# Kernel optimization log

Measured on AMD Instinct MI355X. Metric: run time of the kernel, lower is better.

## Reference

```python
import jax, jax.numpy as jnp
import numpy as np

B, S, D, H = 64, 512, 1024, 1024


def setup_inputs() -> dict:
    key = jax.random.key(0)
    k1, k2, k3 = jax.random.split(key, 3)
    scale = 1.0 / np.sqrt(H)
    U = jax.random.normal(k1, (B, S, D), dtype=jnp.float32)
    W_ih = jax.random.normal(k2, (3 * H, D), dtype=jnp.float32) * scale
    W_hh = jax.random.normal(k3, (3 * H, H), dtype=jnp.float32) * scale
    b_ih = jnp.zeros((3 * H,), dtype=jnp.float32)
    b_hh = jnp.zeros((3 * H,), dtype=jnp.float32)
    return {"U": U, "W_ih": W_ih, "W_hh": W_hh, "b_ih": b_ih, "b_hh": b_hh}


def _gru_scan(U, W_ih, W_hh, b_ih, b_hh):
    # Precompute input-side gate projections for all timesteps: [B,S,3H]
    x_gates = jnp.einsum('bsd,gd->bsg', U, W_ih) + b_ih
    x_gates = jnp.transpose(x_gates, (1, 0, 2))  # [S,B,3H] for scan
    h0 = jnp.zeros((U.shape[0], W_hh.shape[1]), dtype=U.dtype)

    def step(h, xg):
        hg = h @ W_hh.T + b_hh  # [B,3H]
        xr, xz, xn = jnp.split(xg, 3, axis=-1)
        hr, hz, hn = jnp.split(hg, 3, axis=-1)
        r = jax.nn.sigmoid(xr + hr)
        z = jax.nn.sigmoid(xz + hz)
        n = jnp.tanh(xn + r * hn)
        h_new = (1.0 - z) * n + z * h
        return h_new, None

    h_final, _ = jax.lax.scan(step, h0, x_gates)
    return h_final  # [B,H]


def reference(U, W_ih, W_hh, b_ih, b_hh):
    # Dropout p=0.0 (eval-equivalent) -> identity, omitted.
    return _gru_scan(U, W_ih, W_hh, b_ih, b_hh)
```

## Files before the change

### kernel.cpp

```cpp
#include <hip/hip_runtime.h>

#define S_LEN 512
#define BATCH 64
#define HDIM  1024
#define GDIM  3072

typedef __attribute__((ext_vector_type(8))) short bf16x8;
typedef __attribute__((ext_vector_type(4))) float f32x4;
typedef __attribute__((ext_vector_type(4))) unsigned short u16x4;

__device__ inline unsigned short f2bf(float f) {
  unsigned u = __builtin_bit_cast(unsigned, f);
  u += 0x7fffu + ((u >> 16) & 1u);
  return (unsigned short)(u >> 16);
}
__device__ inline float bf2f(unsigned short h) {
  unsigned u = ((unsigned)h) << 16;
  return __builtin_bit_cast(float, u);
}
__device__ inline bf16x8 pack8(float4 a, float4 b) {
  bf16x8 r;
  r[0] = (short)f2bf(a.x); r[1] = (short)f2bf(a.y);
  r[2] = (short)f2bf(a.z); r[3] = (short)f2bf(a.w);
  r[4] = (short)f2bf(b.x); r[5] = (short)f2bf(b.y);
  r[6] = (short)f2bf(b.z); r[7] = (short)f2bf(b.w);
  return r;
}

__global__ __launch_bounds__(256, 2) void xg_gemm(
    const float* __restrict__ U, const float* __restrict__ Wih,
    const float* __restrict__ bih, unsigned short* __restrict__ xg) {
  __shared__ bf16x8 Asub[512];
  __shared__ bf16x8 Bsub[512];

  const int bid = blockIdx.x;
  const int nt = bid % 24;
  const int mt = bid / 24;
  const int tid = threadIdx.x;
  const int wave = tid >> 6, lane = tid & 63;
  const int q = lane >> 4, l15 = lane & 15;
  const int wm = wave >> 1, wn = wave & 1;

  const int srow = tid >> 1, shalf = tid & 1;
  const int arow = mt * 128 + srow;
  const float* Ag = U + ((size_t)(arow & 63) * S_LEN + (arow >> 6)) * HDIM + shalf * 16;
  const float* Bg = Wih + (size_t)(nt * 128 + srow) * HDIM + shalf * 16;
  const int sw = (srow >> 1) & 3;
  const int slot0 = srow * 4 + ((shalf * 2) ^ sw);
  const int slot1 = srow * 4 + ((shalf * 2 + 1) ^ sw);

  f32x4 acc[4][4];
#pragma unroll
  for (int i = 0; i < 4; ++i)
#pragma unroll
    for (int j = 0; j < 4; ++j) acc[i][j] = (f32x4){0.f, 0.f, 0.f, 0.f};

  for (int kk = 0; kk < 32; ++kk) {
    const float4* ap = (const float4*)(Ag + kk * 32);
    float4 a0 = ap[0], a1 = ap[1], a2 = ap[2], a3 = ap[3];
    const float4* bp = (const float4*)(Bg + kk * 32);
    float4 b0 = bp[0], b1 = bp[1], b2 = bp[2], b3 = bp[3];
    Asub[slot0] = pack8(a0, a1);
    Asub[slot1] = pack8(a2, a3);
    Bsub[slot0] = pack8(b0, b1);
    Bsub[slot1] = pack8(b2, b3);
    __syncthreads();
    bf16x8 af[4], bfr[4];
#pragma unroll
    for (int i = 0; i < 4; ++i) {
      int ar = wm * 64 + i * 16 + l15;
      af[i] = Asub[ar * 4 + (q ^ ((ar >> 1) & 3))];
      int br = wn * 64 + i * 16 + l15;
      bfr[i] = Bsub[br * 4 + (q ^ ((br >> 1) & 3))];
    }
#pragma unroll
    for (int i = 0; i < 4; ++i)
#pragma unroll
      for (int j = 0; j < 4; ++j)
        acc[i][j] = __builtin_amdgcn_mfma_f32_16x16x32_bf16(af[i], bfr[j], acc[i][j], 0, 0, 0);
    __syncthreads();
  }

#pragma unroll
  for (int j = 0; j < 4; ++j) {
    int gcol = nt * 128 + wn * 64 + j * 16 + l15;
    float bias = bih[gcol];
#pragma unroll
    for (int i = 0; i < 4; ++i) {
      int rbase = mt * 128 + wm * 64 + i * 16 + q * 4;
      int s = rbase >> 6;
      int b0i = rbase & 63;
      u16x4 pk;
#pragma unroll
      for (int r = 0; r < 4; ++r) pk[r] = f2bf(acc[i][j][r] + bias);
      *(u16x4*)(xg + ((size_t)s * GDIM + gcol) * BATCH + b0i) = pk;
    }
  }
}

__global__ __launch_bounds__(512, 1) void gru_scan(
    const float* __restrict__ Whh, const float* __restrict__ bhh,
    const unsigned short* __restrict__ xg, unsigned short* __restrict__ hbuf,
    unsigned int* __restrict__ flags, float* __restrict__ out) {
  __shared__ unsigned short hls[8 * 8192];
  __shared__ float bh_lds[3][16];

  const int p = blockIdx.x;
  const int j0 = p * 16;
  const int tid = threadIdx.x;
  const int w = tid >> 6, lane = tid & 63;
  const int q = lane >> 4, l15 = lane & 15;
  const int k0 = w * 128;
  const int cb = tid >> 2;
  const int cmq = (tid & 3) * 4;

  const int srow0 = lane >> 4;
  const int sc = lane & 15;

  bf16x8 wf[3][4];
#pragma unroll
  for (int g = 0; g < 3; ++g) {
    const float* wrow = Whh + ((size_t)g * HDIM + j0 + l15) * HDIM + k0;
#pragma unroll
    for (int kk = 0; kk < 4; ++kk) {
      const float4* wp = (const float4*)(wrow + kk * 32 + q * 8);
      wf[g][kk] = pack8(wp[0], wp[1]);
    }
  }
  if (tid < 48) bh_lds[tid >> 4][tid & 15] = bhh[(tid >> 4) * HDIM + j0 + (tid & 15)];
  __syncthreads();

  float4 hv = {0.f, 0.f, 0.f, 0.f};

  unsigned short xq[3][4];
  if (tid < 256) {
#pragma unroll
    for (int g = 0; g < 3; ++g)
#pragma unroll
      for (int r = 0; r < 4; ++r)
        xq[g][r] = xg[((size_t)g * HDIM + j0 + cmq + r) * BATCH + cb];
  }

  const size_t HS = (size_t)BATCH * HDIM;
  int dead = 0;

  for (int t = 0; t < S_LEN; ++t) {
    const unsigned short* hcur = hbuf + (size_t)(t & 1) * HS;
    unsigned short* hnxt = hbuf + (size_t)((t + 1) & 1) * HS;

    {
      const unsigned short* gb = hcur + (size_t)srow0 * HDIM + k0 + sc * 8;
      const unsigned short *g0 = gb,            *g1 = gb + 4 * HDIM,
                           *g2 = gb + 8 * HDIM, *g3 = gb + 12 * HDIM,
                           *g4 = gb + 16 * HDIM,*g5 = gb + 20 * HDIM,
                           *g6 = gb + 24 * HDIM,*g7 = gb + 28 * HDIM;
      bf16x8 v0, v1, v2, v3, v4, v5, v6, v7;
      asm volatile(
          "global_load_dwordx4 %0, %8, off sc0 sc1\n\t"
          "global_load_dwordx4 %1, %9, off sc0 sc1\n\t"
          "global_load_dwordx4 %2, %10, off sc0 sc1\n\t"
          "global_load_dwordx4 %3, %11, off sc0 sc1\n\t"
          "global_load_dwordx4 %4, %12, off sc0 sc1\n\t"
          "global_load_dwordx4 %5, %13, off sc0 sc1\n\t"
          "global_load_dwordx4 %6, %14, off sc0 sc1\n\t"
          "global_load_dwordx4 %7, %15, off sc0 sc1"
          : "=&v"(v0), "=&v"(v1), "=&v"(v2), "=&v"(v3),
            "=&v"(v4), "=&v"(v5), "=&v"(v6), "=&v"(v7)
          : "v"(g0), "v"(g1), "v"(g2), "v"(g3),
            "v"(g4), "v"(g5), "v"(g6), "v"(g7));
      const unsigned short *g8 = gb + 32 * HDIM, *g9 = gb + 36 * HDIM,
                           *gA = gb + 40 * HDIM, *gB = gb + 44 * HDIM,
                           *gC = gb + 48 * HDIM, *gD = gb + 52 * HDIM,
                           *gE = gb + 56 * HDIM, *gF = gb + 60 * HDIM;
      bf16x8 v8, v9, vA, vB, vC, vD, vE, vF;
      asm volatile(
          "global_load_dwordx4 %0, %8, off sc0 sc1\n\t"
          "global_load_dwordx4 %1, %9, off sc0 sc1\n\t"
          "global_load_dwordx4 %2, %10, off sc0 sc1\n\t"
          "global_load_dwordx4 %3, %11, off sc0 sc1\n\t"
          "global_load_dwordx4 %4, %12, off sc0 sc1\n\t"
          "global_load_dwordx4 %5, %13, off sc0 sc1\n\t"
          "global_load_dwordx4 %6, %14, off sc0 sc1\n\t"
          "global_load_dwordx4 %7, %15, off sc0 sc1"
          : "=&v"(v8), "=&v"(v9), "=&v"(vA), "=&v"(vB),
            "=&v"(vC), "=&v"(vD), "=&v"(vE), "=&v"(vF)
          : "v"(g8), "v"(g9), "v"(gA), "v"(gB),
            "v"(gC), "v"(gD), "v"(gE), "v"(gF));

#define STW(J, VV)                                                        \
      {                                                                   \
        const int row_ = srow0 + 4 * (J);                                 \
        const int c2_ = (sc & 8) | ((sc ^ row_) & 7);                     \
        *(bf16x8*)&hls[w * 8192 + row_ * 128 + c2_ * 8] = (VV);           \
      }
      asm volatile("s_waitcnt vmcnt(8)" ::: "memory");
      __builtin_amdgcn_sched_barrier(0);
      STW(0, v0) STW(1, v1) STW(2, v2) STW(3, v3)
      STW(4, v4) STW(5, v5) STW(6, v6) STW(7, v7)
      asm volatile("s_waitcnt vmcnt(0)" ::: "memory");
      __builtin_amdgcn_sched_barrier(0);
      STW(8, v8) STW(9, v9) STW(10, vA) STW(11, vB)
      STW(12, vC) STW(13, vD) STW(14, vE) STW(15, vF)
#undef STW
    }

    f32x4 acc[3][4];
#pragma unroll
    for (int g = 0; g < 3; ++g)
#pragma unroll
      for (int bt = 0; bt < 4; ++bt) acc[g][bt] = (f32x4){0.f, 0.f, 0.f, 0.f};

#pragma unroll
    for (int kk = 0; kk < 4; ++kk) {
      const int c = kk * 4 + q;
      bf16x8 hB[4];
#pragma unroll
      for (int bt = 0; bt < 4; ++bt) {
        const int row = bt * 16 + l15;
        const int c2 = (c & 8) | ((c ^ row) & 7);
        hB[bt] = *(const bf16x8*)&hls[w * 8192 + row * 128 + c2 * 8];
      }
#pragma unroll
      for (int g = 0; g < 3; ++g) {
        acc[g][0] = __builtin_amdgcn_mfma_f32_16x16x32_bf16(wf[g][kk], hB[0], acc[g][0], 0, 0, 0);
        acc[g][1] = __builtin_amdgcn_mfma_f32_16x16x32_bf16(wf[g][kk], hB[1], acc[g][1], 0, 0, 0);
        acc[g][2] = __builtin_amdgcn_mfma_f32_16x16x32_bf16(wf[g][kk], hB[2], acc[g][2], 0, 0, 0);
        acc[g][3] = __builtin_amdgcn_mfma_f32_16x16x32_bf16(wf[g][kk], hB[3], acc[g][3], 0, 0, 0);
      }
    }
    __builtin_amdgcn_sched_barrier(0);

    {
      float* pw = (float*)&hls[w * 8192];
      asm volatile("" : "+v"(pw));
#pragma unroll
      for (int g = 0; g < 3; ++g)
#pragma unroll
        for (int bt = 0; bt < 4; ++bt)
#pragma unroll
          for (int r = 0; r < 4; ++r)
            pw[(g * 16 + q * 4 + r) * 66 + bt * 16 + l15] = acc[g][bt][r];
    }
    __syncthreads();

    if (tid < 256) {
      u16x4 pk;
#pragma unroll
      for (int r = 0; r < 4; ++r) {
        int m = cmq + r;
        float hr = bh_lds[0][m], hz = bh_lds[1][m], hn = bh_lds[2][m];
#pragma unroll
        for (int ww = 0; ww < 8; ++ww) {
          const float* pp = (const float*)&hls[ww * 8192];
          hr += pp[( 0 + m) * 66 + cb];
          hz += pp[(16 + m) * 66 + cb];
          hn += pp[(32 + m) * 66 + cb];
        }
        float xr = bf2f(xq[0][r]), xz = bf2f(xq[1][r]), xn = bf2f(xq[2][r]);
        float rr = 1.f / (1.f + __expf(-(xr + hr)));
        float zz = 1.f / (1.f + __expf(-(xz + hz)));
        float ex = __expf(2.f * (xn + rr * hn));
        float nn = 1.f - 2.f / (ex + 1.f);
        float hold = (r == 0) ? hv.x : (r == 1) ? hv.y : (r == 2) ? hv.z : hv.w;
        float hnew = (1.f - zz) * nn + zz * hold;
        if (r == 0) hv.x = hnew; else if (r == 1) hv.y = hnew; else if (r == 2) hv.z = hnew; else hv.w = hnew;
        pk[r] = f2bf(hnew);
      }
      if (t + 1 < S_LEN) {
        __hip_atomic_store((unsigned long long*)(hnxt + (size_t)cb * HDIM + j0 + cmq),
                           __builtin_bit_cast(unsigned long long, pk),
                           __ATOMIC_RELAXED, __HIP_MEMORY_SCOPE_AGENT);
      }
    }
    __syncthreads();

    if (t + 1 < S_LEN) {
      if (tid == 448)
        __hip_atomic_store(&flags[p], (unsigned)(t + 1),
                           __ATOMIC_RELAXED, __HIP_MEMORY_SCOPE_AGENT);
      if (tid < 256) {
#pragma unroll
        for (int g = 0; g < 3; ++g)
#pragma unroll
          for (int r = 0; r < 4; ++r)
            xq[g][r] = xg[((size_t)(t + 1) * GDIM + g * HDIM + j0 + cmq + r) * BATCH + cb];
      }
      if (tid >= 448 && !dead) {
        const unsigned int* fp = flags + (tid & 63);
        const unsigned want = (unsigned)(t + 1);
        unsigned spins = 0;
        while (__hip_atomic_load(fp, __ATOMIC_RELAXED, __HIP_MEMORY_SCOPE_AGENT)
               < want) {
          __builtin_amdgcn_s_sleep(1);
          if (++spins > 50000000u) { dead = 1; break; }
        }
      }
      __syncthreads();
    }
  }

  if (tid < 256)
    *(float4*)(out + (size_t)cb * HDIM + j0 + cmq) = hv;
}

extern "C" void kernel_launch(void* const* d_in, const int* in_sizes, int n_in,
                              void* d_out, int out_size, void* d_ws, size_t ws_size,
                              hipStream_t stream) {
  const float* U   = (const float*)d_in[0];
  const float* Wih = (const float*)d_in[1];
  const float* Whh = (const float*)d_in[2];
  const float* bih = (const float*)d_in[3];
  const float* bhh = (const float*)d_in[4];
  float* out = (float*)d_out;

  char* ws = (char*)d_ws;
  const size_t XG_BYTES = (size_t)S_LEN * GDIM * BATCH * 2;
  unsigned short* xg   = (unsigned short*)ws;
  unsigned short* hbuf = (unsigned short*)(ws + XG_BYTES);
  const size_t H_BYTES = (size_t)2 * BATCH * HDIM * 2;
  unsigned int* flags  = (unsigned int*)(ws + XG_BYTES + H_BYTES);

  hipMemsetAsync(ws + XG_BYTES, 0, H_BYTES + 256, stream);

  hipLaunchKernelGGL(xg_gemm, dim3((32768 / 128) * (GDIM / 128)), dim3(256), 0, stream,
                     U, Wih, bih, xg);
  hipLaunchKernelGGL(gru_scan, dim3(64), dim3(512), 0, stream,
                     Whh, bhh, xg, hbuf, flags, out);
}
```

Before: 3.595 ms.

## Replace flag-based step barrier with tagged fp32 hidden-state polling

Adds a new scan kernel that keeps the hidden state in fp32 with the step index embedded in the low 8 mantissa bits. Consumers validate each loaded vector's tag and reload until it matches, which removes the separate flag/barrier synchronization between blocks each timestep. This trades twice the hidden-state traffic and a small precision loss in the low mantissa bits for lower inter-block sync latency. The old flag-based kernel stays as a fallback when the workspace is too small.

```diff
diff --git a/kernel.cpp b/kernel.cpp
--- a/kernel.cpp
+++ b/kernel.cpp
@@ -24,6 +24,14 @@
   r[2] = (short)f2bf(a.z); r[3] = (short)f2bf(a.w);
   r[4] = (short)f2bf(b.x); r[5] = (short)f2bf(b.y);
   r[6] = (short)f2bf(b.z); r[7] = (short)f2bf(b.w);
+  return r;
+}
+__device__ inline bf16x8 pack8v(f32x4 a, f32x4 b) {
+  bf16x8 r;
+  r[0] = (short)f2bf(a[0]); r[1] = (short)f2bf(a[1]);
+  r[2] = (short)f2bf(a[2]); r[3] = (short)f2bf(a[3]);
+  r[4] = (short)f2bf(b[0]); r[5] = (short)f2bf(b[1]);
+  r[6] = (short)f2bf(b[2]); r[7] = (short)f2bf(b[3]);
   return r;
 }
 
@@ -98,10 +106,10 @@
   }
 }
 
-__global__ __launch_bounds__(512, 1) void gru_scan(
+__global__ __launch_bounds__(512, 1) void gru_scan_tag(
     const float* __restrict__ Whh, const float* __restrict__ bhh,
-    const unsigned short* __restrict__ xg, unsigned short* __restrict__ hbuf,
-    unsigned int* __restrict__ flags, float* __restrict__ out) {
+    const unsigned short* __restrict__ xg, float* __restrict__ hb32,
+    float* __restrict__ out) {
   __shared__ unsigned short hls[8 * 8192];
   __shared__ float bh_lds[3][16];
 
@@ -131,7 +139,224 @@
   __syncthreads();
 
   float4 hv = {0.f, 0.f, 0.f, 0.f};
-
+  unsigned short xq[3][4];
+
+#define ISSUE8(V0, V1, V2, V3, V4, V5, V6, V7, P0, P1, P2, P3)            \
+  asm volatile(                                                           \
+      "global_load_dwordx4 %0, %8, off sc0 sc1\n\t"                       \
+      "global_load_dwordx4 %1, %8, off offset:16 sc0 sc1\n\t"             \
+      "global_load_dwordx4 %2, %9, off sc0 sc1\n\t"                       \
+      "global_load_dwordx4 %3, %9, off offset:16 sc0 sc1\n\t"             \
+      "global_load_dwordx4 %4, %10, off sc0 sc1\n\t"                      \
+      "global_load_dwordx4 %5, %10, off offset:16 sc0 sc1\n\t"            \
+      "global_load_dwordx4 %6, %11, off sc0 sc1\n\t"                      \
+      "global_load_dwordx4 %7, %11, off offset:16 sc0 sc1"                \
+      : "=&v"(V0), "=&v"(V1), "=&v"(V2), "=&v"(V3),                       \
+        "=&v"(V4), "=&v"(V5), "=&v"(V6), "=&v"(V7)                        \
+      : "v"(P0), "v"(P1), "v"(P2), "v"(P3))
+
+#define CHK(V)                                                            \
+  {                                                                       \
+    unsigned x0 = __builtin_bit_cast(unsigned, (V)[0]);                   \
+    unsigned x1 = __builtin_bit_cast(unsigned, (V)[1]);                   \
+    unsigned x2 = __builtin_bit_cast(unsigned, (V)[2]);                   \
+    unsigned x3 = __builtin_bit_cast(unsigned, (V)[3]);                   \
+    bad |= ((x0 ^ tg) | (x1 ^ tg) | (x2 ^ tg) | (x3 ^ tg)) & 0xffu;       \
+  }
+
+#define VAL8(V0, V1, V2, V3, V4, V5, V6, V7, P0, P1, P2, P3)              \
+  {                                                                       \
+    int rt = 0;                                                           \
+    for (;;) {                                                            \
+      unsigned bad = 0u;                                                  \
+      CHK(V0) CHK(V1) CHK(V2) CHK(V3) CHK(V4) CHK(V5) CHK(V6) CHK(V7)     \
+      if (!__any((int)bad)) break;                                        \
+      if (++rt > 4096) break;      \
+      ISSUE8(V0, V1, V2, V3, V4, V5, V6, V7, P0, P1, P2, P3);             \
+      asm volatile("s_waitcnt vmcnt(0)" ::: "memory");                    \
+      __builtin_amdgcn_sched_barrier(0);                                  \
+    }                                                                     \
+  }
+
+#define STW(J, VA, VB)                                                    \
+  {                                                                       \
+    const int row_ = srow0 + 4 * (J);                                     \
+    const int c2_ = (sc & 8) | ((sc ^ row_) & 7);                         \
+    *(bf16x8*)&hls[w * 8192 + row_ * 128 + c2_ * 8] = pack8v(VA, VB);     \
+  }
+
+  for (int t = 0; t < S_LEN; ++t) {
+    const float* gb_t = hb32 + (size_t)(t & 1) * (BATCH * HDIM);
+    float* gnx = hb32 + (size_t)((t + 1) & 1) * (BATCH * HDIM);
+    const unsigned tg = (unsigned)(t & 0xff);
+
+    {
+      const float* pb = gb_t + (size_t)srow0 * HDIM + k0 + sc * 8;
+      const float *pA0 = pb,               *pA1 = pb + 4 * HDIM,
+                  *pA2 = pb + 8 * HDIM,    *pA3 = pb + 12 * HDIM,
+                  *pB0 = pb + 16 * HDIM,   *pB1 = pb + 20 * HDIM,
+                  *pB2 = pb + 24 * HDIM,   *pB3 = pb + 28 * HDIM,
+                  *pC0 = pb + 32 * HDIM,   *pC1 = pb + 36 * HDIM,
+                  *pC2 = pb + 40 * HDIM,   *pC3 = pb + 44 * HDIM,
+                  *pD0 = pb + 48 * HDIM,   *pD1 = pb + 52 * HDIM,
+                  *pD2 = pb + 56 * HDIM,   *pD3 = pb + 60 * HDIM;
+      f32x4 a0, a1, a2, a3, a4, a5, a6, a7;
+      f32x4 b0, b1, b2, b3, b4, b5, b6, b7;
+      f32x4 c0, c1, c2, c3, c4, c5, c6, c7;
+      f32x4 d0, d1, d2, d3, d4, d5, d6, d7;
+      ISSUE8(a0, a1, a2, a3, a4, a5, a6, a7, pA0, pA1, pA2, pA3);
+      ISSUE8(b0, b1, b2, b3, b4, b5, b6, b7, pB0, pB1, pB2, pB3);
+      ISSUE8(c0, c1, c2, c3, c4, c5, c6, c7, pC0, pC1, pC2, pC3);
+      ISSUE8(d0, d1, d2, d3, d4, d5, d6, d7, pD0, pD1, pD2, pD3);
+
+      asm volatile("s_waitcnt vmcnt(24)" ::: "memory");
+      __builtin_amdgcn_sched_barrier(0);
+      VAL8(a0, a1, a2, a3, a4, a5, a6, a7, pA0, pA1, pA2, pA3);
+      STW(0, a0, a1) STW(1, a2, a3) STW(2, a4, a5) STW(3, a6, a7)
+
+      asm volatile("s_waitcnt vmcnt(16)" ::: "memory");
+      __builtin_amdgcn_sched_barrier(0);
+      VAL8(b0, b1, b2, b3, b4, b5, b6, b7, pB0, pB1, pB2, pB3);
+      STW(4, b0, b1) STW(5, b2, b3) STW(6, b4, b5) STW(7, b6, b7)
+
+      asm volatile("s_waitcnt vmcnt(8)" ::: "memory");
+      __builtin_amdgcn_sched_barrier(0);
+      VAL8(c0, c1, c2, c3, c4, c5, c6, c7, pC0, pC1, pC2, pC3);
+      STW(8, c0, c1) STW(9, c2, c3) STW(10, c4, c5) STW(11, c6, c7)
+
+      asm volatile("s_waitcnt vmcnt(0)" ::: "memory");
+      __builtin_amdgcn_sched_barrier(0);
+      VAL8(d0, d1, d2, d3, d4, d5, d6, d7, pD0, pD1, pD2, pD3);
+      STW(12, d0, d1) STW(13, d2, d3) STW(14, d4, d5) STW(15, d6, d7)
+    }
+
+    if (tid < 256) {
+#pragma unroll
+      for (int g = 0; g < 3; ++g)
+#pragma unroll
+        for (int r = 0; r < 4; ++r)
+          xq[g][r] = xg[((size_t)t * GDIM + g * HDIM + j0 + cmq + r) * BATCH + cb];
+    }
+
+    f32x4 acc[3][4];
+#pragma unroll
+    for (int g = 0; g < 3; ++g)
+#pragma unroll
+      for (int bt = 0; bt < 4; ++bt) acc[g][bt] = (f32x4){0.f, 0.f, 0.f, 0.f};
+
+#pragma unroll
+    for (int kk = 0; kk < 4; ++kk) {
+      const int c = kk * 4 + q;
+      bf16x8 hB[4];
+#pragma unroll
+      for (int bt = 0; bt < 4; ++bt) {
+        const int row = bt * 16 + l15;
+        const int c2 = (c & 8) | ((c ^ row) & 7);
+        hB[bt] = *(const bf16x8*)&hls[w * 8192 + row * 128 + c2 * 8];
+      }
+#pragma unroll
+      for (int g = 0; g < 3; ++g) {
+        acc[g][0] = __builtin_amdgcn_mfma_f32_16x16x32_bf16(wf[g][kk], hB[0], acc[g][0], 0, 0, 0);
+        acc[g][1] = __builtin_amdgcn_mfma_f32_16x16x32_bf16(wf[g][kk], hB[1], acc[g][1], 0, 0, 0);
+        acc[g][2] = __builtin_amdgcn_mfma_f32_16x16x32_bf16(wf[g][kk], hB[2], acc[g][2], 0, 0, 0);
+        acc[g][3] = __builtin_amdgcn_mfma_f32_16x16x32_bf16(wf[g][kk], hB[3], acc[g][3], 0, 0, 0);
+      }
+    }
+    __builtin_amdgcn_sched_barrier(0);
+
+    {
+      float* pw = (float*)&hls[w * 8192];
+      asm volatile("" : "+v"(pw));
+#pragma unroll
+      for (int g = 0; g < 3; ++g)
+#pragma unroll
+        for (int bt = 0; bt < 4; ++bt)
+#pragma unroll
+          for (int r = 0; r < 4; ++r)
+            pw[(g * 16 + q * 4 + r) * 66 + bt * 16 + l15] = acc[g][bt][r];
+    }
+    __syncthreads();
+
+    if (tid < 256) {
+      float hnv[4];
+#pragma unroll
+      for (int r = 0; r < 4; ++r) {
+        int m = cmq + r;
+        float hr = bh_lds[0][m], hz = bh_lds[1][m], hn = bh_lds[2][m];
+#pragma unroll
+        for (int ww = 0; ww < 8; ++ww) {
+          const float* pp = (const float*)&hls[ww * 8192];
+          hr += pp[( 0 + m) * 66 + cb];
+          hz += pp[(16 + m) * 66 + cb];
+          hn += pp[(32 + m) * 66 + cb];
+        }
+        float xr = bf2f(xq[0][r]), xz = bf2f(xq[1][r]), xn = bf2f(xq[2][r]);
+        float rr = 1.f / (1.f + __expf(-(xr + hr)));
+        float zz = 1.f / (1.f + __expf(-(xz + hz)));
+        float ex = __expf(2.f * (xn + rr * hn));
+        float nn = 1.f - 2.f / (ex + 1.f);
+        float hold = (r == 0) ? hv.x : (r == 1) ? hv.y : (r == 2) ? hv.z : hv.w;
+        float hnew = (1.f - zz) * nn + zz * hold;
+        if (r == 0) hv.x = hnew; else if (r == 1) hv.y = hnew; else if (r == 2) hv.z = hnew; else hv.w = hnew;
+        hnv[r] = hnew;
+      }
+      if (t + 1 < S_LEN) {
+        const unsigned tgn = (unsigned)((t + 1) & 0xff);
+        f32x4 st;
+#pragma unroll
+        for (int r = 0; r < 4; ++r) {
+          unsigned u = (__builtin_bit_cast(unsigned, hnv[r]) & 0xffffff00u) | tgn;
+          st[r] = __builtin_bit_cast(float, u);
+        }
+        const float* pst = gnx + (size_t)cb * HDIM + j0 + cmq;
+        asm volatile("global_store_dwordx4 %0, %1, off sc0 sc1"
+                     :: "v"(pst), "v"(st) : "memory");
+      }
+    }
+    __syncthreads();
+  }
+
+#undef ISSUE8
+#undef CHK
+#undef VAL8
+#undef STW
+
+  if (tid < 256)
+    *(float4*)(out + (size_t)cb * HDIM + j0 + cmq) = hv;
+}
+
+__global__ __launch_bounds__(512, 1) void gru_scan_flags(
+    const float* __restrict__ Whh, const float* __restrict__ bhh,
+    const unsigned short* __restrict__ xg, unsigned short* __restrict__ hbuf,
+    unsigned int* __restrict__ flags, float* __restrict__ out) {
+  __shared__ unsigned short hls[8 * 8192];
+  __shared__ float bh_lds[3][16];
+
+  const int p = blockIdx.x;
+  const int j0 = p * 16;
+  const int tid = threadIdx.x;
+  const int w = tid >> 6, lane = tid & 63;
+  const int q = lane >> 4, l15 = lane & 15;
+  const int k0 = w * 128;
+  const int cb = tid >> 2;
+  const int cmq = (tid & 3) * 4;
+  const int srow0 = lane >> 4;
+  const int sc = lane & 15;
+
+  bf16x8 wf[3][4];
+#pragma unroll
+  for (int g = 0; g < 3; ++g) {
+    const float* wrow = Whh + ((size_t)g * HDIM + j0 + l15) * HDIM + k0;
+#pragma unroll
+    for (int kk = 0; kk < 4; ++kk) {
+      const float4* wp = (const float4*)(wrow + kk * 32 + q * 8);
+      wf[g][kk] = pack8(wp[0], wp[1]);
+    }
+  }
+  if (tid < 48) bh_lds[tid >> 4][tid & 15] = bhh[(tid >> 4) * HDIM + j0 + (tid & 15)];
+  __syncthreads();
+
+  float4 hv = {0.f, 0.f, 0.f, 0.f};
   unsigned short xq[3][4];
   if (tid < 256) {
 #pragma unroll
@@ -147,7 +372,6 @@
   for (int t = 0; t < S_LEN; ++t) {
     const unsigned short* hcur = hbuf + (size_t)(t & 1) * HS;
     unsigned short* hnxt = hbuf + (size_t)((t + 1) & 1) * HS;
-
     {
       const unsigned short* gb = hcur + (size_t)srow0 * HDIM + k0 + sc * 8;
       const unsigned short *g0 = gb,            *g1 = gb + 4 * HDIM,
@@ -187,7 +411,7 @@
           : "v"(g8), "v"(g9), "v"(gA), "v"(gB),
             "v"(gC), "v"(gD), "v"(gE), "v"(gF));
 
-#define STW(J, VV)                                                        \
+#define STWF(J, VV)                                                       \
       {                                                                   \
         const int row_ = srow0 + 4 * (J);                                 \
         const int c2_ = (sc & 8) | ((sc ^ row_) & 7);                     \
@@ -195,13 +419,13 @@
       }
       asm volatile("s_waitcnt vmcnt(8)" ::: "memory");
       __builtin_amdgcn_sched_barrier(0);
-      STW(0, v0) STW(1, v1) STW(2, v2) STW(3, v3)
-      STW(4, v4) STW(5, v5) STW(6, v6) STW(7, v7)
+      STWF(0, v0) STWF(1, v1) STWF(2, v2) STWF(3, v3)
+      STWF(4, v4) STWF(5, v5) STWF(6, v6) STWF(7, v7)
       asm volatile("s_waitcnt vmcnt(0)" ::: "memory");
       __builtin_amdgcn_sched_barrier(0);
-      STW(8, v8) STW(9, v9) STW(10, vA) STW(11, vB)
-      STW(12, vC) STW(13, vD) STW(14, vE) STW(15, vF)
-#undef STW
+      STWF(8, v8) STWF(9, v9) STWF(10, vA) STWF(11, vB)
+      STWF(12, vC) STWF(13, vD) STWF(14, vE) STWF(15, vF)
+#undef STWF
     }
 
     f32x4 acc[3][4];
@@ -315,15 +539,23 @@
 
   char* ws = (char*)d_ws;
   const size_t XG_BYTES = (size_t)S_LEN * GDIM * BATCH * 2;
-  unsigned short* xg   = (unsigned short*)ws;
-  unsigned short* hbuf = (unsigned short*)(ws + XG_BYTES);
-  const size_t H_BYTES = (size_t)2 * BATCH * HDIM * 2;
-  unsigned int* flags  = (unsigned int*)(ws + XG_BYTES + H_BYTES);
-
-  hipMemsetAsync(ws + XG_BYTES, 0, H_BYTES + 256, stream);
+  unsigned short* xg = (unsigned short*)ws;
 
   hipLaunchKernelGGL(xg_gemm, dim3((32768 / 128) * (GDIM / 128)), dim3(256), 0, stream,
                      U, Wih, bih, xg);
-  hipLaunchKernelGGL(gru_scan, dim3(64), dim3(512), 0, stream,
-                     Whh, bhh, xg, hbuf, flags, out);
-}
+
+  const size_t H32_BYTES = (size_t)2 * BATCH * HDIM * 4;
+  if (ws_size >= XG_BYTES + H32_BYTES) {
+    float* hb32 = (float*)(ws + XG_BYTES);
+    hipMemsetAsync(ws + XG_BYTES, 0, H32_BYTES, stream);
+    hipLaunchKernelGGL(gru_scan_tag, dim3(64), dim3(512), 0, stream,
+                       Whh, bhh, xg, hb32, out);
+  } else {
+    unsigned short* hbuf = (unsigned short*)(ws + XG_BYTES);
+    const size_t H_BYTES = (size_t)2 * BATCH * HDIM * 2;
+    unsigned int* flags = (unsigned int*)(ws + XG_BYTES + H_BYTES);
+    hipMemsetAsync(ws + XG_BYTES, 0, H_BYTES + 256, stream);
+    hipLaunchKernelGGL(gru_scan_flags, dim3(64), dim3(512), 0, stream,
+                       Whh, bhh, xg, hbuf, flags, out);
+  }
+}
```

Measured after the change: 6.156 ms. 1.71x slower.
